# Performance work log

Hardware: AMD Instinct MI355X
Metric: run time of the kernel (lower is better)

The kernel has to match this reference:

```python
import jax, jax.numpy as jnp
import numpy as np

N = 50000
E = 800000
IN_DIM = 16
HID = 64
HEADS = 4
OUT_DIM = 2
LN_EPS = 1e-5
NEG_SLOPE = 0.2  # GATConv default negative_slope


def _layernorm(h, g, b):
    mu = jnp.mean(h, axis=-1, keepdims=True)
    var = jnp.var(h, axis=-1, keepdims=True)
    return (h - mu) * jax.lax.rsqrt(var + LN_EPS) * g + b


def _gat_layer(h, src, dst, w, a_src, a_dst, b):
    # PyG GATConv, concat=False: per-head channels C=HID, head-averaged output.
    n = h.shape[0]
    xp = (h @ w).reshape(n, HEADS, HID)          # [N,H,C]
    e_src = jnp.sum(xp * a_src, axis=-1)          # [N,H]
    e_dst = jnp.sum(xp * a_dst, axis=-1)          # [N,H]
    e = jax.nn.leaky_relu(e_src[src] + e_dst[dst], negative_slope=NEG_SLOPE)  # [Etot,H]
    # numerically-stable segment softmax over edges grouped by target node
    m = jax.lax.stop_gradient(jax.ops.segment_max(e, dst, num_segments=n))
    ex = jnp.exp(e - m[dst])
    denom = jax.ops.segment_sum(ex, dst, num_segments=n)
    alpha = ex / denom[dst]                       # [Etot,H]
    out = jax.ops.segment_sum(xp[src] * alpha[:, :, None], dst, num_segments=n)  # [N,H,C]
    return jnp.mean(out, axis=1) + b              # mean over heads (concat=False) + bias


def _forward(x, edge_index, w0, a_src0, a_dst0, b0, ln0_g, ln0_b,
             w1, a_src1, a_dst1, b1, ln1_g, ln1_b,
             gru_w_ih, gru_w_hh, gru_b_ih, gru_b_hh,
             d0_w, d0_b, d1_w, d1_b, d2_w, d2_b):
    n = x.shape[0]
    # add_self_loops=True
    loops = jnp.arange(n, dtype=edge_index.dtype)
    src = jnp.concatenate([edge_index[0], loops])
    dst = jnp.concatenate([edge_index[1], loops])
    # GAT layer 1 + LayerNorm + ReLU (dropout is identity in eval)
    h = _gat_layer(x, src, dst, w0, a_src0, a_dst0, b0)
    h = jax.nn.relu(_layernorm(h, ln0_g, ln0_b))
    # GAT layer 2 + LayerNorm (last layer -> no ReLU)
    h = _gat_layer(h, src, dst, w1, a_src1, a_dst1, b1)
    h = _layernorm(h, ln1_g, ln1_b)
    # single-timestep GRU with zero initial hidden state (PyTorch GRU cell math)
    h0 = jnp.zeros((n, HID), dtype=h.dtype)
    gi = h @ gru_w_ih.T + gru_b_ih
    gh = h0 @ gru_w_hh.T + gru_b_hh
    gi_r, gi_z, gi_n = jnp.split(gi, 3, axis=-1)
    gh_r, gh_z, gh_n = jnp.split(gh, 3, axis=-1)
    r = jax.nn.sigmoid(gi_r + gh_r)
    z = jax.nn.sigmoid(gi_z + gh_z)
    cand = jnp.tanh(gi_n + r * gh_n)
    temporal = (1.0 - z) * cand + z * h0
    # MLP decoder on cat([temporal_features, x])
    d = jnp.concatenate([temporal, x], axis=-1)
    d = jax.nn.relu(d @ d0_w + d0_b)
    d = jax.nn.relu(d @ d1_w + d1_b)
    d = d @ d2_w + d2_b
    return jnp.clip(d, -0.5, 0.5)


def setup_inputs():
    key = jax.random.key(0)
    ks = jax.random.split(key, 16)
    rn = lambda k, shape, s=0.05: jax.random.normal(k, shape, dtype=jnp.float32) * s
    return {
        'x': jax.random.normal(ks[0], (N, IN_DIM), dtype=jnp.float32),
        'edge_index': jax.random.randint(ks[1], (2, E), 0, N, dtype=jnp.int32),
        'w0': rn(ks[2], (IN_DIM, HEADS * HID)),
        'a_src0': rn(ks[3], (HEADS, HID)),
        'a_dst0': rn(ks[4], (HEADS, HID)),
        'b0': jnp.zeros((HID,), jnp.float32),
        'ln0_g': jnp.ones((HID,), jnp.float32),
        'ln0_b': jnp.zeros((HID,), jnp.float32),
        'w1': rn(ks[5], (HID, HEADS * HID)),
        'a_src1': rn(ks[6], (HEADS, HID)),
        'a_dst1': rn(ks[7], (HEADS, HID)),
        'b1': jnp.zeros((HID,), jnp.float32),
        'ln1_g': jnp.ones((HID,), jnp.float32),
        'ln1_b': jnp.zeros((HID,), jnp.float32),
        'gru_w_ih': rn(ks[8], (3 * HID, HID)),
        'gru_w_hh': rn(ks[9], (3 * HID, HID)),
        'gru_b_ih': jnp.zeros((3 * HID,), jnp.float32),
        'gru_b_hh': jnp.zeros((3 * HID,), jnp.float32),
        'd0_w': rn(ks[10], (HID + IN_DIM, HID)),
        'd0_b': jnp.zeros((HID,), jnp.float32),
        'd1_w': rn(ks[11], (HID, HID // 2)),
        'd1_b': jnp.zeros((HID // 2,), jnp.float32),
        'd2_w': rn(ks[12], (HID // 2, OUT_DIM)),
        'd2_b': jnp.zeros((OUT_DIM,), jnp.float32),
    }


def reference(x, edge_index, w0, a_src0, a_dst0, b0, ln0_g, ln0_b,
              w1, a_src1, a_dst1, b1, ln1_g, ln1_b,
              gru_w_ih, gru_w_hh, gru_b_ih, gru_b_hh,
              d0_w, d0_b, d1_w, d1_b, d2_w, d2_b):
    return _forward(x, edge_index, w0, a_src0, a_dst0, b0, ln0_g, ln0_b,
                    w1, a_src1, a_dst1, b1, ln1_g, ln1_b,
                    gru_w_ih, gru_w_hh, gru_b_ih, gru_b_hh,
                    d0_w, d0_b, d1_w, d1_b, d2_w, d2_b)
```

## Files before the change

kernel.cpp:

```cpp
#include <hip/hip_runtime.h>
#include <hip/hip_fp16.h>
#include <math.h>

#define NN 50000
#define NE 800000
#define ETOT (NE + NN)
#define HID 64
#define CH 256
#define IND 16
#define LN_EPS 1e-5f
#define NSLOPE 0.2f
#define SCB 49

__device__ __forceinline__ float lrelu(float v){ return v > 0.f ? v : NSLOPE * v; }
__device__ __forceinline__ float sigf(float v){ return 1.f / (1.f + __expf(-v)); }

__device__ __forceinline__ int block_excl_scan(int v, int t, int* wtot){
  const int lane = t & 63, w = t >> 6;
  int inc = v;
  #pragma unroll
  for (int d = 1; d < 64; d <<= 1){
    int tv = __shfl_up(inc, d);
    if (lane >= d) inc += tv;
  }
  if (lane == 63) wtot[w] = inc;
  __syncthreads();
  if (t == 0){
    int acc = 0;
    #pragma unroll
    for (int k = 0; k < 16; ++k){ int tv = wtot[k]; wtot[k] = acc; acc += tv; }
  }
  __syncthreads();
  return wtot[w] + inc - v;
}


__global__ void k_hist(const int* __restrict__ ei, int* __restrict__ deg){
  int e = blockIdx.x * 256 + threadIdx.x;
  if (e >= ETOT) return;
  int d = (e < NE) ? ei[NE + e] : (e - NE);
  atomicAdd(&deg[d], 1);
}

__global__ __launch_bounds__(1024) void k_scan_a(const int* __restrict__ deg,
                                                 int* __restrict__ bsum){
  __shared__ int wtot[16];
  const int t = threadIdx.x, lane = t & 63, w = t >> 6;
  const int i = blockIdx.x * 1024 + t;
  int v = (i < NN) ? deg[i] : 0;
  #pragma unroll
  for (int d = 32; d; d >>= 1) v += __shfl_xor(v, d);
  if (lane == 0) wtot[w] = v;
  __syncthreads();
  if (t == 0){
    int acc = 0;
    #pragma unroll
    for (int k = 0; k < 16; ++k) acc += wtot[k];
    bsum[blockIdx.x] = acc;
  }
}

__global__ __launch_bounds__(64) void k_scan_b(const int* __restrict__ bsum,
                                               int* __restrict__ boff){
  const int t = threadIdx.x;
  int v = (t < SCB) ? bsum[t] : 0;
  int inc = v;
  #pragma unroll
  for (int d = 1; d < 64; d <<= 1){
    int tv = __shfl_up(inc, d);
    if (t >= d) inc += tv;
  }
  if (t < SCB) boff[t] = inc - v;
}

__global__ __launch_bounds__(1024) void k_scan_c(const int* __restrict__ deg,
                                                 const int* __restrict__ boff,
                                                 int* __restrict__ rp,
                                                 int* __restrict__ cursor){
  __shared__ int wtot[16];
  const int t = threadIdx.x;
  const int i = blockIdx.x * 1024 + t;
  int v = (i < NN) ? deg[i] : 0;
  int excl = block_excl_scan(v, t, wtot) + boff[blockIdx.x];
  if (i < NN){ rp[i] = excl; cursor[i] = excl; }
  if (i == NN - 1) rp[NN] = excl + v;
}

__global__ void k_scatter(const int* __restrict__ ei, int* __restrict__ cursor,
                          int* __restrict__ col){
  int e = blockIdx.x * 256 + threadIdx.x;
  if (e >= ETOT) return;
  int s, d;
  if (e < NE){ s = ei[e]; d = ei[NE + e]; } else { s = d = e - NE; }
  int pos = atomicAdd(&cursor[d], 1);
  col[pos] = s;
}


template<int K>
__global__ __launch_bounds__(256) void k_proj(const float* __restrict__ h,
    const float* __restrict__ w, const float* __restrict__ asr,
    const float* __restrict__ adr, __half* __restrict__ xph,
    float* __restrict__ es, float* __restrict__ ed){
  __shared__ float w_s[K * CH];
  __shared__ float h_s[K][36];
  __shared__ float as_s[CH], ad_s[CH];
  const int t = threadIdx.x;
  for (int i = t; i < K * CH; i += 256) w_s[i] = w[i];
  as_s[t] = asr[t]; ad_s[t] = adr[t];
  const int wv = t >> 6, l = t & 63;
  const int tc = l & 31, th = l >> 5;
  const int g = wv * 2 + th;
  const int c0 = tc * 4;
  const int hA = tc >> 4;

  for (int tile = blockIdx.x * 32; tile < NN; tile += gridDim.x * 32){
    __syncthreads();
    for (int i = t; i < 32 * K; i += 256){
      int n = i / K, k = i % K;
      int nn = tile + n;
      h_s[k][n] = (nn < NN) ? h[nn * K + k] : 0.f;
    }
    __syncthreads();

    float acc[4][8];
    #pragma unroll
    for (int j = 0; j < 4; ++j)
      #pragma unroll
      for (int i = 0; i < 8; ++i) acc[j][i] = 0.f;

    #pragma unroll 4
    for (int k = 0; k < K; ++k){
      const float4 wa = *(const float4*)&w_s[k * CH + c0];
      const float4 wb = *(const float4*)&w_s[k * CH + c0 + 128];
      const float4 hv = *(const float4*)&h_s[k][g * 4];
      const float hj0 = hv.x, hj1 = hv.y, hj2 = hv.z, hj3 = hv.w;
      #define STEP(j, hjv) \
        acc[j][0] = fmaf(hjv, wa.x, acc[j][0]); \
        acc[j][1] = fmaf(hjv, wa.y, acc[j][1]); \
        acc[j][2] = fmaf(hjv, wa.z, acc[j][2]); \
        acc[j][3] = fmaf(hjv, wa.w, acc[j][3]); \
        acc[j][4] = fmaf(hjv, wb.x, acc[j][4]); \
        acc[j][5] = fmaf(hjv, wb.y, acc[j][5]); \
        acc[j][6] = fmaf(hjv, wb.z, acc[j][6]); \
        acc[j][7] = fmaf(hjv, wb.w, acc[j][7]);
      STEP(0, hj0) STEP(1, hj1) STEP(2, hj2) STEP(3, hj3)
      #undef STEP
    }

    #pragma unroll
    for (int j = 0; j < 4; ++j){
      const int nj = tile + g * 4 + j;
      float pa = 0.f, pb = 0.f, qa = 0.f, qb = 0.f;
      #pragma unroll
      for (int i = 0; i < 4; ++i){
        pa = fmaf(acc[j][i],     as_s[c0 + i],       pa);
        pb = fmaf(acc[j][4 + i], as_s[c0 + 128 + i], pb);
        qa = fmaf(acc[j][i],     ad_s[c0 + i],       qa);
        qb = fmaf(acc[j][4 + i], ad_s[c0 + 128 + i], qb);
      }
      #pragma unroll
      for (int d = 8; d; d >>= 1){
        pa += __shfl_xor(pa, d); pb += __shfl_xor(pb, d);
        qa += __shfl_xor(qa, d); qb += __shfl_xor(qb, d);
      }
      if (nj < NN){
        union { uint2 u; __half2 h2[2]; } oA, oB;
        oA.h2[0] = __float22half2_rn(make_float2(acc[j][0], acc[j][1]));
        oA.h2[1] = __float22half2_rn(make_float2(acc[j][2], acc[j][3]));
        oB.h2[0] = __float22half2_rn(make_float2(acc[j][4], acc[j][5]));
        oB.h2[1] = __float22half2_rn(make_float2(acc[j][6], acc[j][7]));
        *(uint2*)&xph[(size_t)nj * CH + c0]       = oA.u;
        *(uint2*)&xph[(size_t)nj * CH + c0 + 128] = oB.u;
        if ((tc & 15) == 0){
          es[nj * 4 + hA]     = pa;
          es[nj * 4 + hA + 2] = pb;
          ed[nj * 4 + hA]     = qa;
          ed[nj * 4 + hA + 2] = qb;
        }
      }
    }
  }
}


template<int DO_RELU>
__global__ __launch_bounds__(256) void k_agg(const __half* __restrict__ xph,
    const float4* __restrict__ es4, const float4* __restrict__ ed4,
    const int* __restrict__ rp, const int* __restrict__ col,
    const float* __restrict__ bias, const float* __restrict__ lng,
    const float* __restrict__ lnb, float* __restrict__ hout){
  __shared__ float pbuf[4][2][32][4];
  const int wid = threadIdx.x >> 6, lane = threadIdx.x & 63;
  const int half = lane >> 5, l32 = lane & 31;
  const int n = blockIdx.x * 8 + wid * 2 + half;
  const int head = l32 >> 3;
  const int c8 = l32 * 8;
  const int beg = rp[n];
  const int deg = rp[n + 1] - beg;
  const int dmax = max(deg, __shfl(deg, lane ^ 32));
  const float4 edn = ed4[n];
  float den = 0.f;
  float acc[8];
  #pragma unroll
  for (int i = 0; i < 8; ++i) acc[i] = 0.f;

  for (int base = 0; base < dmax; base += 32){
    const int cmax = min(dmax - base, 32);
    const int myS = col[beg + min(base + l32, deg - 1)];
    const float4 e = es4[myS];
    const bool act = (base + l32 < deg);
    float4 p4;
    p4.x = act ? __expf(lrelu(e.x + edn.x)) : 0.f;
    p4.y = act ? __expf(lrelu(e.y + edn.y)) : 0.f;
    p4.z = act ? __expf(lrelu(e.z + edn.z)) : 0.f;
    p4.w = act ? __expf(lrelu(e.w + edn.w)) : 0.f;
    *(float4*)&pbuf[wid][half][l32][0] = p4;
    const int sOff = myS * CH;

    for (int u0 = 0; u0 < cmax; u0 += 8){
      float pw[8]; uint4 xv[8];
      #pragma unroll
      for (int u = 0; u < 8; ++u){
        const int uu = u0 + u, us = uu & 31;
        const int so = __shfl(sOff, (lane & 32) + us);
        xv[u] = *(const uint4*)&xph[so + c8];
        pw[u] = (uu < cmax) ? pbuf[wid][half][us][head] : 0.f;
      }
      #pragma unroll
      for (int u = 0; u < 8; ++u){
        union { uint4 q; __half2 h2[4]; } cv; cv.q = xv[u];
        const float2 f0 = __half22float2(cv.h2[0]);
        const float2 f1 = __half22float2(cv.h2[1]);
        const float2 f2 = __half22float2(cv.h2[2]);
        const float2 f3 = __half22float2(cv.h2[3]);
        den += pw[u];
        acc[0] = fmaf(f0.x, pw[u], acc[0]); acc[1] = fmaf(f0.y, pw[u], acc[1]);
        acc[2] = fmaf(f1.x, pw[u], acc[2]); acc[3] = fmaf(f1.y, pw[u], acc[3]);
        acc[4] = fmaf(f2.x, pw[u], acc[4]); acc[5] = fmaf(f2.y, pw[u], acc[5]);
        acc[6] = fmaf(f3.x, pw[u], acc[6]); acc[7] = fmaf(f3.y, pw[u], acc[7]);
      }
    }
  }

  const float inv = 1.f / den;
  #pragma unroll
  for (int i = 0; i < 8; ++i) acc[i] *= inv;
  #pragma unroll
  for (int i = 0; i < 8; ++i){
    acc[i] += __shfl_xor(acc[i], 8);
    acc[i] += __shfl_xor(acc[i], 16);
  }
  const int ch0 = (l32 & 7) * 8;
  const float4 bA = *(const float4*)&bias[ch0];
  const float4 bB = *(const float4*)&bias[ch0 + 4];
  acc[0] = acc[0]*0.25f + bA.x; acc[1] = acc[1]*0.25f + bA.y;
  acc[2] = acc[2]*0.25f + bA.z; acc[3] = acc[3]*0.25f + bA.w;
  acc[4] = acc[4]*0.25f + bB.x; acc[5] = acc[5]*0.25f + bB.y;
  acc[6] = acc[6]*0.25f + bB.z; acc[7] = acc[7]*0.25f + bB.w;
  float s = 0.f, q = 0.f;
  #pragma unroll
  for (int i = 0; i < 8; ++i){ s += acc[i]; q += acc[i]*acc[i]; }
  #pragma unroll
  for (int d = 4; d; d >>= 1){ s += __shfl_xor(s, d); q += __shfl_xor(q, d); }
  const float mu = s * (1.f / 64.f);
  const float var = q * (1.f / 64.f) - mu * mu;
  const float rs = rsqrtf(var + LN_EPS);
  const float4 gA = *(const float4*)&lng[ch0];
  const float4 gB = *(const float4*)&lng[ch0 + 4];
  const float4 tA = *(const float4*)&lnb[ch0];
  const float4 tB = *(const float4*)&lnb[ch0 + 4];
  acc[0] = (acc[0]-mu)*rs*gA.x + tA.x; acc[1] = (acc[1]-mu)*rs*gA.y + tA.y;
  acc[2] = (acc[2]-mu)*rs*gA.z + tA.z; acc[3] = (acc[3]-mu)*rs*gA.w + tA.w;
  acc[4] = (acc[4]-mu)*rs*gB.x + tB.x; acc[5] = (acc[5]-mu)*rs*gB.y + tB.y;
  acc[6] = (acc[6]-mu)*rs*gB.z + tB.z; acc[7] = (acc[7]-mu)*rs*gB.w + tB.w;
  if (DO_RELU){
    #pragma unroll
    for (int i = 0; i < 8; ++i) acc[i] = fmaxf(acc[i], 0.f);
  }
  if (l32 < 8){
    float4 oA, oB;
    oA.x = acc[0]; oA.y = acc[1]; oA.z = acc[2]; oA.w = acc[3];
    oB.x = acc[4]; oB.y = acc[5]; oB.z = acc[6]; oB.w = acc[7];
    *(float4*)&hout[n * HID + l32 * 8]     = oA;
    *(float4*)&hout[n * HID + l32 * 8 + 4] = oB;
  }
}


__global__ __launch_bounds__(256) void k_head(const float* __restrict__ h,
    const float* __restrict__ x, const float* __restrict__ wih,
    const float* __restrict__ bih, const float* __restrict__ bhh,
    const float* __restrict__ d0w, const float* __restrict__ d0b,
    const float* __restrict__ d1w, const float* __restrict__ d1b,
    const float* __restrict__ d2w, const float* __restrict__ d2b,
    float* __restrict__ out){
  __shared__ __half wT[64 * 196];
  __shared__ __half w0s[80 * 64];
  __shared__ __half w1s[64 * 32];
  __shared__ float w2s[64];
  __shared__ float bi_s[192], bh_s[192], b0s[64], b1s[32], b2s[2];
  __shared__ float h_s[64][34];
  __shared__ float dc[80][34];
  __shared__ float t0s[64][34];
  __shared__ float t1s[32][34];
  const int t = threadIdx.x;
  for (int i = t; i < 192 * 64; i += 256)
    wT[(i & 63) * 196 + (i >> 6)] = __float2half(wih[i]);
  for (int i = t; i < 80 * 64; i += 256) w0s[i] = __float2half(d0w[i]);
  for (int i = t; i < 64 * 32; i += 256) w1s[i] = __float2half(d1w[i]);
  if (t < 64) w2s[t] = d2w[t];
  if (t < 192){ bi_s[t] = bih[t]; bh_s[t] = bhh[t]; }
  if (t < 64) b0s[t] = d0b[t];
  if (t < 32) b1s[t] = d1b[t];
  if (t < 2)  b2s[t] = d2b[t];

  const int tile = blockIdx.x * 32;
  for (int i = t; i < 32 * 64; i += 256){
    int nidx = i >> 6, k = i & 63;
    int nn = tile + nidx;
    h_s[k][nidx] = (nn < NN) ? h[nn * 64 + k] : 0.f;
  }
  for (int i = t; i < 32 * 16; i += 256){
    int nidx = i >> 4, k = i & 15;
    int nn = tile + nidx;
    dc[64 + k][nidx] = (nn < NN) ? x[nn * IND + k] : 0.f;
  }
  __syncthreads();

  const int col = t & 15, gg = t >> 4, c0 = col * 4;
  {
    float ar[2][4] = {{0}}, az[2][4] = {{0}}, an[2][4] = {{0}};
    #pragma unroll 4
    for (int k = 0; k < 64; ++k){
      union { uint2 u; __half2 h2[2]; } R, Z, N_;
      R.u  = *(const uint2*)&wT[k * 196 + c0];
      Z.u  = *(const uint2*)&wT[k * 196 + 64 + c0];
      N_.u = *(const uint2*)&wT[k * 196 + 128 + c0];
      const float2 r01 = __half22float2(R.h2[0]),  r23 = __half22float2(R.h2[1]);
      const float2 z01 = __half22float2(Z.h2[0]),  z23 = __half22float2(Z.h2[1]);
      const float2 n01 = __half22float2(N_.h2[0]), n23 = __half22float2(N_.h2[1]);
      const float h0v = h_s[k][gg * 2];
      const float h1v = h_s[k][gg * 2 + 1];
      ar[0][0] = fmaf(h0v, r01.x, ar[0][0]); ar[0][1] = fmaf(h0v, r01.y, ar[0][1]);
      ar[0][2] = fmaf(h0v, r23.x, ar[0][2]); ar[0][3] = fmaf(h0v, r23.y, ar[0][3]);
      az[0][0] = fmaf(h0v, z01.x, az[0][0]); az[0][1] = fmaf(h0v, z01.y, az[0][1]);
      az[0][2] = fmaf(h0v, z23.x, az[0][2]); az[0][3] = fmaf(h0v, z23.y, az[0][3]);
      an[0][0] = fmaf(h0v, n01.x, an[0][0]); an[0][1] = fmaf(h0v, n01.y, an[0][1]);
      an[0][2] = fmaf(h0v, n23.x, an[0][2]); an[0][3] = fmaf(h0v, n23.y, an[0][3]);
      ar[1][0] = fmaf(h1v, r01.x, ar[1][0]); ar[1][1] = fmaf(h1v, r01.y, ar[1][1]);
      ar[1][2] = fmaf(h1v, r23.x, ar[1][2]); ar[1][3] = fmaf(h1v, r23.y, ar[1][3]);
      az[1][0] = fmaf(h1v, z01.x, az[1][0]); az[1][1] = fmaf(h1v, z01.y, az[1][1]);
      az[1][2] = fmaf(h1v, z23.x, az[1][2]); az[1][3] = fmaf(h1v, z23.y, az[1][3]);
      an[1][0] = fmaf(h1v, n01.x, an[1][0]); an[1][1] = fmaf(h1v, n01.y, an[1][1]);
      an[1][2] = fmaf(h1v, n23.x, an[1][2]); an[1][3] = fmaf(h1v, n23.y, an[1][3]);
    }
    #pragma unroll
    for (int j = 0; j < 2; ++j){
      #pragma unroll
      for (int i = 0; i < 4; ++i){
        const int c = c0 + i;
        const float r  = sigf(ar[j][i] + bi_s[c] + bh_s[c]);
        const float zz = sigf(az[j][i] + bi_s[64 + c] + bh_s[64 + c]);
        const float cd = tanhf(an[j][i] + bi_s[128 + c] + r * bh_s[128 + c]);
        dc[c][gg * 2 + j] = (1.f - zz) * cd;
      }
    }
  }
  __syncthreads();

  {
    float a[2][4] = {{0}};
    #pragma unroll 4
    for (int k = 0; k < 80; ++k){
      union { uint2 u; __half2 h2[2]; } W;
      W.u = *(const uint2*)&w0s[k * 64 + c0];
      const float2 w01 = __half22float2(W.h2[0]), w23 = __half22float2(W.h2[1]);
      const float b0v = dc[k][gg * 2];
      const float b1v = dc[k][gg * 2 + 1];
      a[0][0] = fmaf(b0v, w01.x, a[0][0]); a[0][1] = fmaf(b0v, w01.y, a[0][1]);
      a[0][2] = fmaf(b0v, w23.x, a[0][2]); a[0][3] = fmaf(b0v, w23.y, a[0][3]);
      a[1][0] = fmaf(b1v, w01.x, a[1][0]); a[1][1] = fmaf(b1v, w01.y, a[1][1]);
      a[1][2] = fmaf(b1v, w23.x, a[1][2]); a[1][3] = fmaf(b1v, w23.y, a[1][3]);
    }
    #pragma unroll
    for (int j = 0; j < 2; ++j)
      #pragma unroll
      for (int i = 0; i < 4; ++i)
        t0s[c0 + i][gg * 2 + j] = fmaxf(a[j][i] + b0s[c0 + i], 0.f);
  }
  __syncthreads();

  {
    const int c1 = (t & 7) * 4, g1 = t >> 3;
    float a[4] = {0, 0, 0, 0};
    #pragma unroll 4
    for (int k = 0; k < 64; ++k){
      union { uint2 u; __half2 h2[2]; } W;
      W.u = *(const uint2*)&w1s[k * 32 + c1];
      const float2 w01 = __half22float2(W.h2[0]), w23 = __half22float2(W.h2[1]);
      const float bv = t0s[k][g1];
      a[0] = fmaf(bv, w01.x, a[0]); a[1] = fmaf(bv, w01.y, a[1]);
      a[2] = fmaf(bv, w23.x, a[2]); a[3] = fmaf(bv, w23.y, a[3]);
    }
    #pragma unroll
    for (int i = 0; i < 4; ++i)
      t1s[c1 + i][g1] = fmaxf(a[i] + b1s[c1 + i], 0.f);
  }
  __syncthreads();

  if (t < 64){
    const int nidx = t >> 1, o = t & 1;
    float a = b2s[o];
    #pragma unroll
    for (int k = 0; k < 32; ++k) a = fmaf(t1s[k][nidx], w2s[k * 2 + o], a);
    const int nn = tile + nidx;
    if (nn < NN) out[nn * 2 + o] = fminf(fmaxf(a, -0.5f), 0.5f);
  }
}


extern "C" void kernel_launch(void* const* d_in, const int* in_sizes, int n_in,
                              void* d_out, int out_size, void* d_ws, size_t ws_size,
                              hipStream_t stream){
  (void)in_sizes; (void)n_in; (void)out_size; (void)ws_size;
  const float* x      = (const float*)d_in[0];
  const int*   ei     = (const int*)d_in[1];
  const float* w0     = (const float*)d_in[2];
  const float* as0    = (const float*)d_in[3];
  const float* ad0    = (const float*)d_in[4];
  const float* b0     = (const float*)d_in[5];
  const float* ln0g   = (const float*)d_in[6];
  const float* ln0b   = (const float*)d_in[7];
  const float* w1     = (const float*)d_in[8];
  const float* as1    = (const float*)d_in[9];
  const float* ad1    = (const float*)d_in[10];
  const float* b1     = (const float*)d_in[11];
  const float* ln1g   = (const float*)d_in[12];
  const float* ln1b   = (const float*)d_in[13];
  const float* wih    = (const float*)d_in[14];
  const float* bih    = (const float*)d_in[16];
  const float* bhh    = (const float*)d_in[17];
  const float* d0w    = (const float*)d_in[18];
  const float* d0b    = (const float*)d_in[19];
  const float* d1w    = (const float*)d_in[20];
  const float* d1b    = (const float*)d_in[21];
  const float* d2w    = (const float*)d_in[22];
  const float* d2b    = (const float*)d_in[23];
  float* outp = (float*)d_out;

  char* ws = (char*)d_ws;
  size_t o = 0;
  auto alloc = [&](size_t bytes) -> char* {
    char* r = ws + o;
    o += (bytes + 255) & ~(size_t)255;
    return r;
  };
  int*    deg    = (int*)   alloc(NN * sizeof(int));
  int*    rp     = (int*)   alloc((NN + 1) * sizeof(int));
  int*    cursor = (int*)   alloc(NN * sizeof(int));
  int*    col    = (int*)   alloc((size_t)ETOT * sizeof(int));
  int*    bsum   = (int*)   alloc(SCB * sizeof(int));
  int*    boff   = (int*)   alloc(SCB * sizeof(int));
  float*  es     = (float*) alloc((size_t)NN * 4 * sizeof(float));
  float*  ed     = (float*) alloc((size_t)NN * 4 * sizeof(float));
  __half* xph    = (__half*)alloc((size_t)NN * CH * sizeof(__half));
  float*  hbuf   = (float*) alloc((size_t)NN * HID * sizeof(float));

  hipMemsetAsync(deg, 0, NN * sizeof(int), stream);
  k_hist<<<(ETOT + 255) / 256, 256, 0, stream>>>(ei, deg);
  k_scan_a<<<SCB, 1024, 0, stream>>>(deg, bsum);
  k_scan_b<<<1, 64, 0, stream>>>(bsum, boff);
  k_scan_c<<<SCB, 1024, 0, stream>>>(deg, boff, rp, cursor);
  k_scatter<<<(ETOT + 255) / 256, 256, 0, stream>>>(ei, cursor, col);
  k_proj<IND><<<(NN + 31) / 32, 256, 0, stream>>>(x, w0, as0, ad0, xph, es, ed);
  k_agg<1><<<NN / 8, 256, 0, stream>>>(xph, (const float4*)es, (const float4*)ed,
                                       rp, col, b0, ln0g, ln0b, hbuf);
  k_proj<HID><<<(NN + 31) / 32, 256, 0, stream>>>(hbuf, w1, as1, ad1, xph, es, ed);
  k_agg<0><<<NN / 8, 256, 0, stream>>>(xph, (const float4*)es, (const float4*)ed,
                                       rp, col, b1, ln1g, ln1b, hbuf);
  k_head<<<(NN + 31) / 32, 256, 0, stream>>>(hbuf, x, wih, bih, bhh,
                                             d0w, d0b, d1w, d1b, d2w, d2b, outp);
}
```

Baseline: 349.8 us.

## Store layer-2 projection weights as fp16 in LDS and split head into GRU and decoder kernels

```diff
diff --git a/kernel.cpp b/kernel.cpp
--- a/kernel.cpp
+++ b/kernel.cpp
@@ -97,16 +97,21 @@
 }
 
 
-template<int K>
+template<int K, bool WHALF>
 __global__ __launch_bounds__(256) void k_proj(const float* __restrict__ h,
     const float* __restrict__ w, const float* __restrict__ asr,
     const float* __restrict__ adr, __half* __restrict__ xph,
     float* __restrict__ es, float* __restrict__ ed){
-  __shared__ float w_s[K * CH];
+  __shared__ float  w_sf[WHALF ? 1 : K * CH];
+  __shared__ __half w_sh[WHALF ? K * CH : 1];
   __shared__ float h_s[K][36];
   __shared__ float as_s[CH], ad_s[CH];
   const int t = threadIdx.x;
-  for (int i = t; i < K * CH; i += 256) w_s[i] = w[i];
+  if (WHALF){
+    for (int i = t; i < K * CH; i += 256) w_sh[i] = __float2half(w[i]);
+  } else {
+    for (int i = t; i < K * CH; i += 256) w_sf[i] = w[i];
+  }
   as_s[t] = asr[t]; ad_s[t] = adr[t];
   const int wv = t >> 6, l = t & 63;
   const int tc = l & 31, th = l >> 5;
@@ -131,8 +136,19 @@
 
     #pragma unroll 4
     for (int k = 0; k < K; ++k){
-      const float4 wa = *(const float4*)&w_s[k * CH + c0];
-      const float4 wb = *(const float4*)&w_s[k * CH + c0 + 128];
+      float4 wa, wb;
+      if (WHALF){
+        union { uint2 u; __half2 h2[2]; } A, B;
+        A.u = *(const uint2*)&w_sh[k * CH + c0];
+        B.u = *(const uint2*)&w_sh[k * CH + c0 + 128];
+        const float2 a01 = __half22float2(A.h2[0]), a23 = __half22float2(A.h2[1]);
+        const float2 b01 = __half22float2(B.h2[0]), b23 = __half22float2(B.h2[1]);
+        wa.x = a01.x; wa.y = a01.y; wa.z = a23.x; wa.w = a23.y;
+        wb.x = b01.x; wb.y = b01.y; wb.z = b23.x; wb.w = b23.y;
+      } else {
+        wa = *(const float4*)&w_sf[k * CH + c0];
+        wb = *(const float4*)&w_sf[k * CH + c0 + 128];
+      }
       const float4 hv = *(const float4*)&h_s[k][g * 4];
       const float hj0 = hv.x, hj1 = hv.y, hj2 = hv.z, hj3 = hv.w;
       #define STEP(j, hjv) \
@@ -288,55 +304,37 @@
 }
 
 
-__global__ __launch_bounds__(256) void k_head(const float* __restrict__ h,
-    const float* __restrict__ x, const float* __restrict__ wih,
-    const float* __restrict__ bih, const float* __restrict__ bhh,
-    const float* __restrict__ d0w, const float* __restrict__ d0b,
-    const float* __restrict__ d1w, const float* __restrict__ d1b,
-    const float* __restrict__ d2w, const float* __restrict__ d2b,
-    float* __restrict__ out){
-  __shared__ __half wT[64 * 196];
-  __shared__ __half w0s[80 * 64];
-  __shared__ __half w1s[64 * 32];
-  __shared__ float w2s[64];
-  __shared__ float bi_s[192], bh_s[192], b0s[64], b1s[32], b2s[2];
+#define WTS 196
+
+__global__ __launch_bounds__(256) void k_gru(const float* __restrict__ h,
+    const float* __restrict__ wih, const float* __restrict__ bih,
+    const float* __restrict__ bhh, float* __restrict__ tmp){
+  __shared__ __half wT[64 * WTS];
   __shared__ float h_s[64][34];
-  __shared__ float dc[80][34];
-  __shared__ float t0s[64][34];
-  __shared__ float t1s[32][34];
+  __shared__ float bi_s[192], bh_s[192];
   const int t = threadIdx.x;
   for (int i = t; i < 192 * 64; i += 256)
-    wT[(i & 63) * 196 + (i >> 6)] = __float2half(wih[i]);
-  for (int i = t; i < 80 * 64; i += 256) w0s[i] = __float2half(d0w[i]);
-  for (int i = t; i < 64 * 32; i += 256) w1s[i] = __float2half(d1w[i]);
-  if (t < 64) w2s[t] = d2w[t];
+    wT[(i & 63) * WTS + (i >> 6)] = __float2half(wih[i]);
   if (t < 192){ bi_s[t] = bih[t]; bh_s[t] = bhh[t]; }
-  if (t < 64) b0s[t] = d0b[t];
-  if (t < 32) b1s[t] = d1b[t];
-  if (t < 2)  b2s[t] = d2b[t];
-
-  const int tile = blockIdx.x * 32;
-  for (int i = t; i < 32 * 64; i += 256){
-    int nidx = i >> 6, k = i & 63;
-    int nn = tile + nidx;
-    h_s[k][nidx] = (nn < NN) ? h[nn * 64 + k] : 0.f;
-  }
-  for (int i = t; i < 32 * 16; i += 256){
-    int nidx = i >> 4, k = i & 15;
-    int nn = tile + nidx;
-    dc[64 + k][nidx] = (nn < NN) ? x[nn * IND + k] : 0.f;
-  }
-  __syncthreads();
-
-  const int col = t & 15, gg = t >> 4, c0 = col * 4;
-  {
+  const int col = t & 15, gg = t >> 4;
+  const int c0 = col * 4;
+
+  for (int tile = blockIdx.x * 32; tile < NN; tile += gridDim.x * 32){
+    __syncthreads();
+    for (int i = t; i < 32 * 64; i += 256){
+      int nidx = i >> 6, k = i & 63;
+      int nn = tile + nidx;
+      h_s[k][nidx] = (nn < NN) ? h[nn * 64 + k] : 0.f;
+    }
+    __syncthreads();
+
     float ar[2][4] = {{0}}, az[2][4] = {{0}}, an[2][4] = {{0}};
     #pragma unroll 4
     for (int k = 0; k < 64; ++k){
       union { uint2 u; __half2 h2[2]; } R, Z, N_;
-      R.u  = *(const uint2*)&wT[k * 196 + c0];
-      Z.u  = *(const uint2*)&wT[k * 196 + 64 + c0];
-      N_.u = *(const uint2*)&wT[k * 196 + 128 + c0];
+      R.u  = *(const uint2*)&wT[k * WTS + c0];
+      Z.u  = *(const uint2*)&wT[k * WTS + 64 + c0];
+      N_.u = *(const uint2*)&wT[k * WTS + 128 + c0];
       const float2 r01 = __half22float2(R.h2[0]),  r23 = __half22float2(R.h2[1]);
       const float2 z01 = __half22float2(Z.h2[0]),  z23 = __half22float2(Z.h2[1]);
       const float2 n01 = __half22float2(N_.h2[0]), n23 = __half22float2(N_.h2[1]);
@@ -355,67 +353,111 @@
       an[1][0] = fmaf(h1v, n01.x, an[1][0]); an[1][1] = fmaf(h1v, n01.y, an[1][1]);
       an[1][2] = fmaf(h1v, n23.x, an[1][2]); an[1][3] = fmaf(h1v, n23.y, an[1][3]);
     }
+
     #pragma unroll
     for (int j = 0; j < 2; ++j){
-      #pragma unroll
-      for (int i = 0; i < 4; ++i){
-        const int c = c0 + i;
-        const float r  = sigf(ar[j][i] + bi_s[c] + bh_s[c]);
-        const float zz = sigf(az[j][i] + bi_s[64 + c] + bh_s[64 + c]);
-        const float cd = tanhf(an[j][i] + bi_s[128 + c] + r * bh_s[128 + c]);
-        dc[c][gg * 2 + j] = (1.f - zz) * cd;
-      }
-    }
-  }
-  __syncthreads();
-
-  {
-    float a[2][4] = {{0}};
-    #pragma unroll 4
-    for (int k = 0; k < 80; ++k){
-      union { uint2 u; __half2 h2[2]; } W;
-      W.u = *(const uint2*)&w0s[k * 64 + c0];
-      const float2 w01 = __half22float2(W.h2[0]), w23 = __half22float2(W.h2[1]);
-      const float b0v = dc[k][gg * 2];
-      const float b1v = dc[k][gg * 2 + 1];
-      a[0][0] = fmaf(b0v, w01.x, a[0][0]); a[0][1] = fmaf(b0v, w01.y, a[0][1]);
-      a[0][2] = fmaf(b0v, w23.x, a[0][2]); a[0][3] = fmaf(b0v, w23.y, a[0][3]);
-      a[1][0] = fmaf(b1v, w01.x, a[1][0]); a[1][1] = fmaf(b1v, w01.y, a[1][1]);
-      a[1][2] = fmaf(b1v, w23.x, a[1][2]); a[1][3] = fmaf(b1v, w23.y, a[1][3]);
-    }
-    #pragma unroll
-    for (int j = 0; j < 2; ++j)
+      const int nj = tile + gg * 2 + j;
+      if (nj < NN){
+        float tv[4];
+        #pragma unroll
+        for (int i = 0; i < 4; ++i){
+          const int c = c0 + i;
+          const float r  = sigf(ar[j][i] + bi_s[c] + bh_s[c]);
+          const float zz = sigf(az[j][i] + bi_s[64 + c] + bh_s[64 + c]);
+          const float cd = tanhf(an[j][i] + bi_s[128 + c] + r * bh_s[128 + c]);
+          tv[i] = (1.f - zz) * cd;
+        }
+        float4 o; o.x = tv[0]; o.y = tv[1]; o.z = tv[2]; o.w = tv[3];
+        *(float4*)&tmp[(size_t)nj * 64 + c0] = o;
+      }
+    }
+  }
+}
+
+
+__global__ __launch_bounds__(256) void k_dec(const float* __restrict__ tmp,
+    const float* __restrict__ x, const float* __restrict__ d0w,
+    const float* __restrict__ d0b, const float* __restrict__ d1w,
+    const float* __restrict__ d1b, const float* __restrict__ d2w,
+    const float* __restrict__ d2b, float* __restrict__ out){
+  __shared__ __half w0s[80 * 64];
+  __shared__ __half w1s[64 * 32];
+  __shared__ float w2s[64];
+  __shared__ float b0s[64], b1s[32], b2s[2];
+  __shared__ float dc[80][34];
+  __shared__ float t0s[64][34];
+  __shared__ float t1s[32][34];
+  const int t = threadIdx.x;
+  for (int i = t; i < 80 * 64; i += 256) w0s[i] = __float2half(d0w[i]);
+  for (int i = t; i < 64 * 32; i += 256) w1s[i] = __float2half(d1w[i]);
+  if (t < 64) w2s[t] = d2w[t];
+  if (t < 64) b0s[t] = d0b[t];
+  if (t < 32) b1s[t] = d1b[t];
+  if (t < 2)  b2s[t] = d2b[t];
+
+  for (int tile = blockIdx.x * 32; tile < NN; tile += gridDim.x * 32){
+    __syncthreads();
+    for (int i = t; i < 32 * 64; i += 256){
+      int nidx = i >> 6, k = i & 63;
+      int nn = tile + nidx;
+      dc[k][nidx] = (nn < NN) ? tmp[(size_t)nn * 64 + k] : 0.f;
+    }
+    for (int i = t; i < 32 * 16; i += 256){
+      int nidx = i >> 4, k = i & 15;
+      int nn = tile + nidx;
+      dc[64 + k][nidx] = (nn < NN) ? x[nn * IND + k] : 0.f;
+    }
+    __syncthreads();
+
+    {
+      const int col = t & 15, gg = t >> 4, c0 = col * 4;
+      float a[2][4] = {{0}};
+      #pragma unroll 4
+      for (int k = 0; k < 80; ++k){
+        union { uint2 u; __half2 h2[2]; } W;
+        W.u = *(const uint2*)&w0s[k * 64 + c0];
+        const float2 w01 = __half22float2(W.h2[0]), w23 = __half22float2(W.h2[1]);
+        const float b0v = dc[k][gg * 2];
+        const float b1v = dc[k][gg * 2 + 1];
+        a[0][0] = fmaf(b0v, w01.x, a[0][0]); a[0][1] = fmaf(b0v, w01.y, a[0][1]);
+        a[0][2] = fmaf(b0v, w23.x, a[0][2]); a[0][3] = fmaf(b0v, w23.y, a[0][3]);
+        a[1][0] = fmaf(b1v, w01.x, a[1][0]); a[1][1] = fmaf(b1v, w01.y, a[1][1]);
+        a[1][2] = fmaf(b1v, w23.x, a[1][2]); a[1][3] = fmaf(b1v, w23.y, a[1][3]);
+      }
+      #pragma unroll
+      for (int j = 0; j < 2; ++j)
+        #pragma unroll
+        for (int i = 0; i < 4; ++i)
+          t0s[c0 + i][gg * 2 + j] = fmaxf(a[j][i] + b0s[c0 + i], 0.f);
+    }
+    __syncthreads();
+
+    {
+      const int c1 = (t & 7) * 4, g1 = t >> 3;
+      float a[4] = {0, 0, 0, 0};
+      #pragma unroll 4
+      for (int k = 0; k < 64; ++k){
+        union { uint2 u; __half2 h2[2]; } W;
+        W.u = *(const uint2*)&w1s[k * 32 + c1];
+        const float2 w01 = __half22float2(W.h2[0]), w23 = __half22float2(W.h2[1]);
+        const float bv = t0s[k][g1];
+        a[0] = fmaf(bv, w01.x, a[0]); a[1] = fmaf(bv, w01.y, a[1]);
+        a[2] = fmaf(bv, w23.x, a[2]); a[3] = fmaf(bv, w23.y, a[3]);
+      }
       #pragma unroll
       for (int i = 0; i < 4; ++i)
-        t0s[c0 + i][gg * 2 + j] = fmaxf(a[j][i] + b0s[c0 + i], 0.f);
-  }
-  __syncthreads();
-
-  {
-    const int c1 = (t & 7) * 4, g1 = t >> 3;
-    float a[4] = {0, 0, 0, 0};
-    #pragma unroll 4
-    for (int k = 0; k < 64; ++k){
-      union { uint2 u; __half2 h2[2]; } W;
-      W.u = *(const uint2*)&w1s[k * 32 + c1];
-      const float2 w01 = __half22float2(W.h2[0]), w23 = __half22float2(W.h2[1]);
-      const float bv = t0s[k][g1];
-      a[0] = fmaf(bv, w01.x, a[0]); a[1] = fmaf(bv, w01.y, a[1]);
-      a[2] = fmaf(bv, w23.x, a[2]); a[3] = fmaf(bv, w23.y, a[3]);
-    }
-    #pragma unroll
-    for (int i = 0; i < 4; ++i)
-      t1s[c1 + i][g1] = fmaxf(a[i] + b1s[c1 + i], 0.f);
-  }
-  __syncthreads();
-
-  if (t < 64){
-    const int nidx = t >> 1, o = t & 1;
-    float a = b2s[o];
-    #pragma unroll
-    for (int k = 0; k < 32; ++k) a = fmaf(t1s[k][nidx], w2s[k * 2 + o], a);
-    const int nn = tile + nidx;
-    if (nn < NN) out[nn * 2 + o] = fminf(fmaxf(a, -0.5f), 0.5f);
+        t1s[c1 + i][g1] = fmaxf(a[i] + b1s[c1 + i], 0.f);
+    }
+    __syncthreads();
+
+    if (t < 64){
+      const int nidx = t >> 1, o = t & 1;
+      float a = b2s[o];
+      #pragma unroll
+      for (int k = 0; k < 32; ++k) a = fmaf(t1s[k][nidx], w2s[k * 2 + o], a);
+      const int nn = tile + nidx;
+      if (nn < NN) out[nn * 2 + o] = fminf(fmaxf(a, -0.5f), 0.5f);
+    }
   }
 }
 
@@ -466,6 +508,7 @@
   float*  ed     = (float*) alloc((size_t)NN * 4 * sizeof(float));
   __half* xph    = (__half*)alloc((size_t)NN * CH * sizeof(__half));
   float*  hbuf   = (float*) alloc((size_t)NN * HID * sizeof(float));
+  float*  tmp    = (float*) alloc((size_t)NN * HID * sizeof(float));
 
   hipMemsetAsync(deg, 0, NN * sizeof(int), stream);
   k_hist<<<(ETOT + 255) / 256, 256, 0, stream>>>(ei, deg);
@@ -473,12 +516,15 @@
   k_scan_b<<<1, 64, 0, stream>>>(bsum, boff);
   k_scan_c<<<SCB, 1024, 0, stream>>>(deg, boff, rp, cursor);
   k_scatter<<<(ETOT + 255) / 256, 256, 0, stream>>>(ei, cursor, col);
-  k_proj<IND><<<(NN + 31) / 32, 256, 0, stream>>>(x, w0, as0, ad0, xph, es, ed);
+  k_proj<IND, false><<<(NN + 31) / 32, 256, 0, stream>>>(x, w0, as0, ad0,
+                                                         xph, es, ed);
   k_agg<1><<<NN / 8, 256, 0, stream>>>(xph, (const float4*)es, (const float4*)ed,
                                        rp, col, b0, ln0g, ln0b, hbuf);
-  k_proj<HID><<<(NN + 31) / 32, 256, 0, stream>>>(hbuf, w1, as1, ad1, xph, es, ed);
+  k_proj<HID, true><<<(NN + 31) / 32, 256, 0, stream>>>(hbuf, w1, as1, ad1,
+                                                        xph, es, ed);
   k_agg<0><<<NN / 8, 256, 0, stream>>>(xph, (const float4*)es, (const float4*)ed,
                                        rp, col, b1, ln1g, ln1b, hbuf);
-  k_head<<<(NN + 31) / 32, 256, 0, stream>>>(hbuf, x, wih, bih, bhh,
-                                             d0w, d0b, d1w, d1b, d2w, d2b, outp);
-}
+  k_gru<<<(NN + 31) / 32, 256, 0, stream>>>(hbuf, wih, bih, bhh, tmp);
+  k_dec<<<(NN + 31) / 32, 256, 0, stream>>>(tmp, x, d0w, d0b, d1w, d1b, d2w, d2b,
+                                            outp);
+}
```

Measured after the change: 346.5 us. No clear change (-0.9%).
